# Optimization experiments

Measured on AMD Instinct MI355X. Metric: run time of the kernel, lower is better.

The kernel has to match this reference:

```python
import jax, jax.numpy as jnp
import numpy as np

B, T, F, H, A = 256, 256, 512, 1024, 1000
EPS = 1e-7  # keras CategoricalCrossentropy clip epsilon


def setup_inputs() -> dict:
    key = jax.random.key(0)
    ks = jax.random.split(key, 8)
    sF, sH = 1.0 / np.sqrt(F), 1.0 / np.sqrt(H)
    return {
        "inputs": jax.random.normal(ks[0], (B, T, F), dtype=jnp.float32),
        "Wx": jax.random.normal(ks[1], (F, H), dtype=jnp.float32) * sF,
        "Wh": jax.random.normal(ks[2], (H, H), dtype=jnp.float32) * sH,
        "b_rnn": jnp.zeros((H,), dtype=jnp.float32),
        "W1": jax.random.normal(ks[3], (H, H), dtype=jnp.float32) * sH,
        "b1": jnp.zeros((H,), dtype=jnp.float32),
        "W2": jax.random.normal(ks[4], (H, A), dtype=jnp.float32) * sH,
        "b2": jnp.zeros((A,), dtype=jnp.float32),
    }


def reference(inputs, Wx, Wh, b_rnn, W1, b1, W2, b2):
    # SimpleRNN with relu: h_t = relu(x_t @ Wx + h_{t-1} @ Wh + b)
    # Precompute the input projection as one big GEMM, then scan the recurrence.
    xw = jnp.einsum("btf,fh->bth", inputs, Wx) + b_rnn  # [B,T,H]

    def step(h, xw_t):
        h_new = jax.nn.relu(xw_t + h @ Wh)
        return h_new, None

    h0 = jnp.zeros((inputs.shape[0], Wh.shape[0]), dtype=inputs.dtype)
    h_last, _ = jax.lax.scan(step, h0, jnp.swapaxes(xw, 0, 1))  # scan over time

    hid = jax.nn.relu(h_last @ W1 + b1)                 # Dense relu
    probs = jax.nn.softmax(hid @ W2 + b2, axis=-1)      # Dense softmax -> [B,A]

    # tf.random.categorical receives the softmax *probabilities* but treats them
    # as unnormalized log-probs; we reproduce that faithfully with a fixed key.
    action = jax.random.categorical(jax.random.key(42), probs, axis=-1)
    action = action.astype(jnp.int32)

    # CategoricalCrossentropy(one_hot(action), probs), mean over batch
    targets = jax.nn.one_hot(action, probs.shape[-1], dtype=probs.dtype)
    p = jnp.clip(probs, EPS, 1.0 - EPS)
    loss = -jnp.mean(jnp.sum(targets * jnp.log(p), axis=-1))
    return action, loss
```

## Files before the change

kernel.cpp:

```cpp
#include <hip/hip_runtime.h>
#include <hip/hip_bf16.h>

#define B_ 256
#define T_ 256
#define F_ 512
#define H_ 1024
#define A_ 1000
#define EPS_ 1e-7f

typedef __hip_bfloat16 bf16;

__global__ __launch_bounds__(256) void detect_kernel(
    const unsigned* __restrict__ wx_words, int* __restrict__ flag)
{
    __shared__ int cnt[256];
    const int tid = threadIdx.x;
    int c = 0;
    for (int k = tid; k < 65536; k += 256) {
        unsigned lo = wx_words[k] & 0xFFFFu;
        unsigned e = (lo >> 7) & 0xFFu;
        if (e >= 105u && e <= 126u) c++;
    }
    cnt[tid] = c;
    __syncthreads();
    for (int s = 128; s > 0; s >>= 1) {
        if (tid < s) cnt[tid] += cnt[tid + s];
        __syncthreads();
    }
    if (tid == 0) flag[0] = (cnt[0] > 32768) ? 1 : 0;
}

__device__ __forceinline__ float load_maybe(const void* p, long i, int isbf16)
{
    return isbf16 ? __bfloat162float(((const bf16*)p)[i])
                  : ((const float*)p)[i];
}

__global__ __launch_bounds__(256) void gemm_kernel(
    const void* __restrict__ A1, int a1_maybe, long a1_off, int lda1, int K1,
    const float* __restrict__ A2, int lda2, int K2,
    const void* __restrict__ Wa, const void* __restrict__ Wb,
    const void* __restrict__ bias,
    const int* __restrict__ flagp,
    float* __restrict__ C, int M, int N, int do_relu)
{
    const int flagv = flagp[0];
    const int a1_bf = a1_maybe ? flagv : 0;

    __shared__ float As[32][33];
    __shared__ float Bs[32][33];

    const int tid = threadIdx.x;
    const int tx = tid & 15;
    const int ty = tid >> 4;
    const int n0 = blockIdx.x * 32;
    const int m0 = blockIdx.y * 32;

    float acc00 = 0.f, acc01 = 0.f, acc10 = 0.f, acc11 = 0.f;

    for (int part = 0; part < 2; ++part) {
        const void* Wp = part ? Wb : Wa;
        const int    K = part ? K2 : K1;
        if (part == 1 && (A2 == nullptr || K2 <= 0)) continue;

        for (int k0 = 0; k0 < K; k0 += 32) {
            #pragma unroll
            for (int i = 0; i < 4; ++i) {
                int idx = tid + i * 256;
                int r = idx >> 5, c = idx & 31;
                float av;
                if (part == 0) {
                    long off = a1_off + (long)(m0 + r) * lda1 + (k0 + c);
                    av = load_maybe(A1, off, a1_bf);
                } else {
                    av = A2[(long)(m0 + r) * lda2 + (k0 + c)];
                }
                As[r][c] = av;
                int n = n0 + c;
                Bs[r][c] = (n < N) ? load_maybe(Wp, (long)(k0 + r) * N + n, flagv)
                                   : 0.0f;
            }
            __syncthreads();
            #pragma unroll
            for (int k = 0; k < 32; ++k) {
                float a0 = As[ty * 2][k];
                float a1 = As[ty * 2 + 1][k];
                float b0 = Bs[k][tx * 2];
                float b1 = Bs[k][tx * 2 + 1];
                acc00 = fmaf(a0, b0, acc00); acc01 = fmaf(a0, b1, acc01);
                acc10 = fmaf(a1, b0, acc10); acc11 = fmaf(a1, b1, acc11);
            }
            __syncthreads();
        }
    }

    const int m = m0 + ty * 2;
    const int n = n0 + tx * 2;
    float bs0 = (n     < N) ? load_maybe(bias, n,     flagv) : 0.0f;
    float bs1 = (n + 1 < N) ? load_maybe(bias, n + 1, flagv) : 0.0f;
    float v00 = acc00 + bs0, v01 = acc01 + bs1;
    float v10 = acc10 + bs0, v11 = acc11 + bs1;
    if (do_relu) {
        v00 = fmaxf(v00, 0.f); v01 = fmaxf(v01, 0.f);
        v10 = fmaxf(v10, 0.f); v11 = fmaxf(v11, 0.f);
    }
    if (n     < N) C[(long)m * N + n]           = v00;
    if (n + 1 < N) C[(long)m * N + n + 1]       = v01;
    if (n     < N) C[(long)(m + 1) * N + n]     = v10;
    if (n + 1 < N) C[(long)(m + 1) * N + n + 1] = v11;
}

__global__ __launch_bounds__(256, 2) void xw_gemm_kernel(
    const void* __restrict__ X,
    const void* __restrict__ Wx,
    const void* __restrict__ brnn,
    const int* __restrict__ flagp,
    float* __restrict__ C,
    int t0)
{
    const int flagv = flagp[0];
    __shared__ float As[16][132];
    __shared__ float Bs[16][132];

    const int tid = threadIdx.x;
    const int tx = tid & 15;
    const int ty = tid >> 4;
    const int n0 = blockIdx.x * 128;
    const int m0 = blockIdx.y * 128;

    float acc[8][8] = {{0.f}};

    for (int k0 = 0; k0 < F_; k0 += 16) {
        #pragma unroll
        for (int i = 0; i < 8; ++i) {
            int idx = tid + i * 256;
            int ka = idx & 15, r = idx >> 4;
            int rg = m0 + r;
            long irow = (long)(rg >> 5) * 256 + t0 + (rg & 31);
            As[ka][r] = load_maybe(X, irow * F_ + k0 + ka, flagv);
            int nb = idx & 127, kb = idx >> 7;
            Bs[kb][nb] = load_maybe(Wx, (long)(k0 + kb) * H_ + n0 + nb, flagv);
        }
        __syncthreads();
        #pragma unroll
        for (int k = 0; k < 16; ++k) {
            float4 a0 = *(const float4*)&As[k][ty * 4];
            float4 a1 = *(const float4*)&As[k][ty * 4 + 64];
            float4 b0 = *(const float4*)&Bs[k][tx * 4];
            float4 b1 = *(const float4*)&Bs[k][tx * 4 + 64];
            float av[8] = {a0.x, a0.y, a0.z, a0.w, a1.x, a1.y, a1.z, a1.w};
            float bv[8] = {b0.x, b0.y, b0.z, b0.w, b1.x, b1.y, b1.z, b1.w};
            #pragma unroll
            for (int i = 0; i < 8; ++i)
                #pragma unroll
                for (int j = 0; j < 8; ++j)
                    acc[i][j] = fmaf(av[i], bv[j], acc[i][j]);
        }
        __syncthreads();
    }

    float bb[8];
    #pragma unroll
    for (int j = 0; j < 8; ++j) {
        int n = n0 + tx * 4 + (j & 3) + (j >> 2) * 64;
        bb[j] = load_maybe(brnn, n, flagv);
    }
    #pragma unroll
    for (int i = 0; i < 8; ++i) {
        int m = m0 + ty * 4 + (i & 3) + (i >> 2) * 64;
        float4 v0 = {acc[i][0] + bb[0], acc[i][1] + bb[1],
                     acc[i][2] + bb[2], acc[i][3] + bb[3]};
        float4 v1 = {acc[i][4] + bb[4], acc[i][5] + bb[5],
                     acc[i][6] + bb[6], acc[i][7] + bb[7]};
        *(float4*)&C[(long)m * H_ + n0 + tx * 4]      = v0;
        *(float4*)&C[(long)m * H_ + n0 + tx * 4 + 64] = v1;
    }
}

__global__ __launch_bounds__(256) void convert_wh_kernel(
    const void* __restrict__ Wh, const int* __restrict__ flagp,
    float* __restrict__ whf)
{
    const int flagv = flagp[0];
    long i = (long)blockIdx.x * 256 + threadIdx.x;
    whf[i] = load_maybe(Wh, i, flagv);
}

__global__ __launch_bounds__(1024) void rnn_step2_kernel(
    const float* __restrict__ hT,
    const float* __restrict__ Wh,
    const float* __restrict__ xw,
    float* __restrict__ hTn)
{
    const int tid  = threadIdx.x;
    const int lane = tid & 63;
    const int w    = __builtin_amdgcn_readfirstlane(tid >> 6);
    const int g    = w & 3;
    const int q    = w >> 2;
    const int m    = blockIdx.y * 64 + lane;
    const int n0   = blockIdx.x * 16 + g * 4;

    const float* __restrict__ ap = hT + ((long)q << 16) + m;
    const float* __restrict__ bp = Wh + ((long)q << 18) + n0;

    float acc0 = 0.f, acc1 = 0.f, acc2 = 0.f, acc3 = 0.f;
    #pragma unroll 8
    for (int k = 0; k < 256; ++k) {
        float  a = ap[(long)k << 8];
        float4 b = *(const float4*)(bp + ((long)k << 10));
        acc0 = fmaf(a, b.x, acc0);
        acc1 = fmaf(a, b.y, acc1);
        acc2 = fmaf(a, b.z, acc2);
        acc3 = fmaf(a, b.w, acc3);
    }

    __shared__ float4 part[3][4][64];
    if (q > 0) part[q - 1][g][lane] = make_float4(acc0, acc1, acc2, acc3);
    __syncthreads();

    if (q == 0) {
        float4 p0 = part[0][g][lane];
        float4 p1 = part[1][g][lane];
        float4 p2 = part[2][g][lane];
        const float4 xv = *(const float4*)(xw + (long)m * (32 * 1024) + n0);
        float s0 = ((acc0 + p0.x) + p1.x) + p2.x;
        float s1 = ((acc1 + p0.y) + p1.y) + p2.y;
        float s2 = ((acc2 + p0.z) + p1.z) + p2.z;
        float s3 = ((acc3 + p0.w) + p1.w) + p2.w;
        float v0 = fmaxf(s0 + xv.x, 0.f);
        float v1 = fmaxf(s1 + xv.y, 0.f);
        float v2 = fmaxf(s2 + xv.z, 0.f);
        float v3 = fmaxf(s3 + xv.w, 0.f);
        hTn[(long)(n0 + 0) * 256 + m] = v0;
        hTn[(long)(n0 + 1) * 256 + m] = v1;
        hTn[(long)(n0 + 2) * 256 + m] = v2;
        hTn[(long)(n0 + 3) * 256 + m] = v3;
    }
}

__global__ __launch_bounds__(256) void transpose_kernel(
    const float* __restrict__ in,
    float* __restrict__ out)
{
    __shared__ float t[32][33];
    const int tid = threadIdx.x;
    const int c  = tid & 31;
    const int r8 = tid >> 5;
    const int x0 = blockIdx.x * 32;
    const int y0 = blockIdx.y * 32;
    #pragma unroll
    for (int i = 0; i < 4; ++i) {
        int r = r8 + i * 8;
        t[r][c] = in[(long)(x0 + r) * 256 + y0 + c];
    }
    __syncthreads();
    #pragma unroll
    for (int i = 0; i < 4; ++i) {
        int r = r8 + i * 8;
        out[(long)(y0 + r) * 1024 + x0 + c] = t[c][r];
    }
}

__device__ __forceinline__ unsigned rotl32(unsigned v, int r) {
    return (v << r) | (v >> (32 - r));
}

__device__ __forceinline__ void threefry2x32(unsigned k0, unsigned k1,
                                             unsigned x0, unsigned x1,
                                             unsigned& o0, unsigned& o1)
{
    unsigned ks2 = k0 ^ k1 ^ 0x1BD11BDAu;
    x0 += k0; x1 += k1;
#define R4(ra, rb, rc, rd)                              \
    x0 += x1; x1 = rotl32(x1, ra); x1 ^= x0;            \
    x0 += x1; x1 = rotl32(x1, rb); x1 ^= x0;            \
    x0 += x1; x1 = rotl32(x1, rc); x1 ^= x0;            \
    x0 += x1; x1 = rotl32(x1, rd); x1 ^= x0;
    R4(13, 15, 26, 6);  x0 += k1;  x1 += ks2 + 1u;
    R4(17, 29, 16, 24); x0 += ks2; x1 += k0  + 2u;
    R4(13, 15, 26, 6);  x0 += k0;  x1 += k1  + 3u;
    R4(17, 29, 16, 24); x0 += k1;  x1 += ks2 + 4u;
    R4(13, 15, 26, 6);  x0 += ks2; x1 += k0  + 5u;
#undef R4
    o0 = x0; o1 = x1;
}

__device__ __forceinline__ float gumbel_at(unsigned j)
{
    unsigned o0, o1;
    threefry2x32(0u, 42u, 0u, j, o0, o1);
    unsigned bits = o0 ^ o1;
    unsigned ub = (bits >> 9) | 0x3F800000u;
    float u = __uint_as_float(ub) - 1.0f;
    const float TINY = 1.1754943508222875e-38f;
    u = fmaxf(TINY, u * (1.0f - TINY) + TINY);
    return -logf(-logf(u));
}

__global__ __launch_bounds__(256) void sample_kernel(
    const float* __restrict__ logits,
    float* __restrict__ out,
    float* __restrict__ loss_acc)
{
    const int b = blockIdx.x;
    const int tid = threadIdx.x;
    const float* row = logits + (long)b * A_;

    __shared__ float sv[256];
    __shared__ int   si[256];

    float lv[4];
    float lmax = -INFINITY;
    #pragma unroll
    for (int i = 0; i < 4; ++i) {
        int a = tid + i * 256;
        lv[i] = (a < A_) ? row[a] : -INFINITY;
        lmax = fmaxf(lmax, lv[i]);
    }
    sv[tid] = lmax;
    __syncthreads();
    for (int s = 128; s > 0; s >>= 1) {
        if (tid < s) sv[tid] = fmaxf(sv[tid], sv[tid + s]);
        __syncthreads();
    }
    lmax = sv[0];
    __syncthreads();

    float e[4];
    float lsum = 0.f;
    #pragma unroll
    for (int i = 0; i < 4; ++i) {
        int a = tid + i * 256;
        e[i] = (a < A_) ? expf(lv[i] - lmax) : 0.0f;
        lsum += e[i];
    }
    sv[tid] = lsum;
    __syncthreads();
    for (int s = 128; s > 0; s >>= 1) {
        if (tid < s) sv[tid] += sv[tid + s];
        __syncthreads();
    }
    const float inv = 1.0f / sv[0];
    __syncthreads();

    float bestv = -INFINITY;
    int   besti = 500;
    #pragma unroll
    for (int i = 0; i < 4; ++i) {
        int a = tid + i * 256;
        if (a < A_) {
            float score = e[i] * inv + gumbel_at((unsigned)(b * A_ + a));
            if (score > bestv) { bestv = score; besti = a; }
        }
    }
    sv[tid] = bestv; si[tid] = besti;
    __syncthreads();
    for (int s = 128; s > 0; s >>= 1) {
        if (tid < s) {
            float v2 = sv[tid + s]; int i2 = si[tid + s];
            if (v2 > sv[tid] || (v2 == sv[tid] && i2 < si[tid])) {
                sv[tid] = v2; si[tid] = i2;
            }
        }
        __syncthreads();
    }

    if (tid == 0) {
        int act = si[0];
        out[b] = (float)act;
        float p = expf(row[act] - lmax) * inv;
        p = fminf(fmaxf(p, EPS_), 1.0f - EPS_);
        atomicAdd(loss_acc, -logf(p) * (1.0f / (float)B_));
    }
}

__global__ void finalize_kernel(const float* __restrict__ loss_acc,
                                float* __restrict__ out)
{
    out[B_] = *loss_acc;
}

extern "C" void kernel_launch(void* const* d_in, const int* in_sizes, int n_in,
                              void* d_out, int out_size, void* d_ws, size_t ws_size,
                              hipStream_t stream)
{
    (void)out_size;

    const void *inputs = nullptr, *Wx = nullptr, *Wh = nullptr, *b_rnn = nullptr,
               *W1 = nullptr, *b1 = nullptr, *W2 = nullptr, *b2 = nullptr;
    for (int i = 0; i < n_in; ++i) {
        int s = in_sizes[i];
        if      (s == 33554432) inputs = d_in[i];
        else if (s == 524288)   Wx = d_in[i];
        else if (s == 1048576)  { if (!Wh) Wh = d_in[i]; else W1 = d_in[i]; }
        else if (s == 1024)     { if (!b_rnn) b_rnn = d_in[i]; else b1 = d_in[i]; }
        else if (s == 1024000)  W2 = d_in[i];
        else if (s == 1000)     b2 = d_in[i];
    }
    if (!inputs) inputs = d_in[0];
    if (!Wx) Wx = d_in[1];  if (!Wh) Wh = d_in[2];  if (!b_rnn) b_rnn = d_in[3];
    if (!W1) W1 = d_in[4];  if (!b1) b1 = d_in[5];  if (!W2) W2 = d_in[6];
    if (!b2) b2 = d_in[7];

    float* out = (float*)d_out;
    float* ws = (float*)d_ws;

    dim3 blk(256);
    dim3 grdH((H_ + 31) / 32, B_ / 32);
    dim3 grdA((A_ + 31) / 32, B_ / 32);

    const size_t XW_FLOATS = (size_t)8192 * 1024;
    const size_t need_floats = XW_FLOATS + 2 * 262144 + 1048576
                             + 262144 + 262144 + 256000 + 2;
    if (ws_size >= need_floats * sizeof(float)) {
        float* xwbuf    = ws;
        float* hT0      = xwbuf + XW_FLOATS;
        float* hT1      = hT0 + 262144;
        float* whf      = hT1 + 262144;
        float* hlast    = whf + 1048576;
        float* hid      = hlast + 262144;
        float* logits   = hid + 262144;
        float* loss_acc = logits + 256000;
        int*   flag     = (int*)(loss_acc + 1);

        hipMemsetAsync(hT0, 0, 262144 * sizeof(float), stream);
        hipMemsetAsync(loss_acc, 0, sizeof(float), stream);

        detect_kernel<<<1, blk, 0, stream>>>((const unsigned*)Wx, flag);
        convert_wh_kernel<<<4096, blk, 0, stream>>>(Wh, flag, whf);

        float* hp = hT0;
        float* hn = hT1;
        for (int c = 0; c < 8; ++c) {
            xw_gemm_kernel<<<dim3(8, 64), blk, 0, stream>>>(
                inputs, Wx, b_rnn, flag, xwbuf, c * 32);
            for (int tl = 0; tl < 32; ++tl) {
                rnn_step2_kernel<<<dim3(64, 4), dim3(1024), 0, stream>>>(
                    hp, whf, xwbuf + (long)tl * 1024, hn);
                float* tmp = hp; hp = hn; hn = tmp;
            }
        }

        transpose_kernel<<<dim3(32, 8), blk, 0, stream>>>(hp, hlast);

        gemm_kernel<<<grdH, blk, 0, stream>>>(
            hlast, 0, 0, H_, H_, nullptr, 0, 0, W1, nullptr, b1, flag,
            hid, B_, H_, 1);
        gemm_kernel<<<grdA, blk, 0, stream>>>(
            hid, 0, 0, H_, H_, nullptr, 0, 0, W2, nullptr, b2, flag,
            logits, B_, A_, 0);

        sample_kernel<<<dim3(B_), blk, 0, stream>>>(logits, out, loss_acc);
        finalize_kernel<<<1, 1, 0, stream>>>(loss_acc, out);
        return;
    }

    float* hA       = ws;
    float* hB       = hA + (long)B_ * H_;
    float* hid      = hB + (long)B_ * H_;
    float* logits   = hid + (long)B_ * H_;
    float* loss_acc = logits + (long)B_ * A_;
    int*   flag     = (int*)(loss_acc + 1);

    hipMemsetAsync(hA, 0, (size_t)B_ * H_ * sizeof(float), stream);
    hipMemsetAsync(loss_acc, 0, sizeof(float), stream);

    detect_kernel<<<1, blk, 0, stream>>>((const unsigned*)Wx, flag);

    float* hp = hA;
    float* hn = hB;
    for (int t = 0; t < T_; ++t) {
        gemm_kernel<<<grdH, blk, 0, stream>>>(
            inputs, 1, (long)t * F_, T_ * F_, F_,
            hp, H_, H_,
            Wx, Wh, b_rnn, flag,
            hn, B_, H_, 1);
        float* tmp = hp; hp = hn; hn = tmp;
    }

    gemm_kernel<<<grdH, blk, 0, stream>>>(
        hp, 0, 0, H_, H_, nullptr, 0, 0, W1, nullptr, b1, flag, hid, B_, H_, 1);
    gemm_kernel<<<grdA, blk, 0, stream>>>(
        hid, 0, 0, H_, H_, nullptr, 0, 0, W2, nullptr, b2, flag, logits, B_, A_, 0);

    sample_kernel<<<dim3(B_), blk, 0, stream>>>(logits, out, loss_acc);
    finalize_kernel<<<1, 1, 0, stream>>>(loss_acc, out);
}
```

Before: 5.401 ms.

## Restructure RNN step kernel to split K across 16 waves with wider batch tiles

Replaces the per-step recurrence kernel with a variant in which each block covers 64 hidden outputs by 16 batch rows. The K dimension is split across 16 wavefronts of 64 each, so every thread keeps 16 accumulators and loads one Wh value per k, with the hidden-state values broadcast as float4s. Partial sums are reduced through shared memory, then bias, ReLU and the transposed store are applied. The aim is to raise FMA-to-load ratio and Wh reuse per step, at the cost of a 16-way shared-memory reduction and a strided global write.

Measured after the change: 7.078 ms. 31.1% more time.

```diff
diff --git a/kernel.cpp b/kernel.cpp
--- a/kernel.cpp
+++ b/kernel.cpp
@@ -186,56 +186,71 @@
     whf[i] = load_maybe(Wh, i, flagv);
 }
 
-__global__ __launch_bounds__(1024) void rnn_step2_kernel(
+__global__ __launch_bounds__(1024) void rnn_step3_kernel(
     const float* __restrict__ hT,
     const float* __restrict__ Wh,
     const float* __restrict__ xw,
     float* __restrict__ hTn)
 {
+    __shared__ float part[16][64][16];
+
     const int tid  = threadIdx.x;
     const int lane = tid & 63;
-    const int w    = __builtin_amdgcn_readfirstlane(tid >> 6);
-    const int g    = w & 3;
-    const int q    = w >> 2;
-    const int m    = blockIdx.y * 64 + lane;
-    const int n0   = blockIdx.x * 16 + g * 4;
-
-    const float* __restrict__ ap = hT + ((long)q << 16) + m;
-    const float* __restrict__ bp = Wh + ((long)q << 18) + n0;
-
-    float acc0 = 0.f, acc1 = 0.f, acc2 = 0.f, acc3 = 0.f;
-    #pragma unroll 8
-    for (int k = 0; k < 256; ++k) {
-        float  a = ap[(long)k << 8];
-        float4 b = *(const float4*)(bp + ((long)k << 10));
-        acc0 = fmaf(a, b.x, acc0);
-        acc1 = fmaf(a, b.y, acc1);
-        acc2 = fmaf(a, b.z, acc2);
-        acc3 = fmaf(a, b.w, acc3);
-    }
-
-    __shared__ float4 part[3][4][64];
-    if (q > 0) part[q - 1][g][lane] = make_float4(acc0, acc1, acc2, acc3);
-    __syncthreads();
-
-    if (q == 0) {
-        float4 p0 = part[0][g][lane];
-        float4 p1 = part[1][g][lane];
-        float4 p2 = part[2][g][lane];
-        const float4 xv = *(const float4*)(xw + (long)m * (32 * 1024) + n0);
-        float s0 = ((acc0 + p0.x) + p1.x) + p2.x;
-        float s1 = ((acc1 + p0.y) + p1.y) + p2.y;
-        float s2 = ((acc2 + p0.z) + p1.z) + p2.z;
-        float s3 = ((acc3 + p0.w) + p1.w) + p2.w;
-        float v0 = fmaxf(s0 + xv.x, 0.f);
-        float v1 = fmaxf(s1 + xv.y, 0.f);
-        float v2 = fmaxf(s2 + xv.z, 0.f);
-        float v3 = fmaxf(s3 + xv.w, 0.f);
-        hTn[(long)(n0 + 0) * 256 + m] = v0;
-        hTn[(long)(n0 + 1) * 256 + m] = v1;
-        hTn[(long)(n0 + 2) * 256 + m] = v2;
-        hTn[(long)(n0 + 3) * 256 + m] = v3;
-    }
+    const int q    = __builtin_amdgcn_readfirstlane(tid >> 6);
+    const int n    = blockIdx.x * 64 + lane;
+    const int m0   = blockIdx.y * 16;
+
+    const float* __restrict__ wp = Wh + ((long)q << 6) * H_ + n;
+    const float* __restrict__ hp = hT + ((long)q << 6) * B_ + m0;
+
+    float acc[16];
+    #pragma unroll
+    for (int i = 0; i < 16; ++i) acc[i] = 0.f;
+
+    #pragma unroll 4
+    for (int k = 0; k < 64; ++k) {
+        float wv = wp[(long)k << 10];
+        const float4* hv = (const float4*)(hp + ((long)k << 8));
+        float4 h0 = hv[0];
+        float4 h1 = hv[1];
+        float4 h2 = hv[2];
+        float4 h3 = hv[3];
+        acc[0]  = fmaf(h0.x, wv, acc[0]);
+        acc[1]  = fmaf(h0.y, wv, acc[1]);
+        acc[2]  = fmaf(h0.z, wv, acc[2]);
+        acc[3]  = fmaf(h0.w, wv, acc[3]);
+        acc[4]  = fmaf(h1.x, wv, acc[4]);
+        acc[5]  = fmaf(h1.y, wv, acc[5]);
+        acc[6]  = fmaf(h1.z, wv, acc[6]);
+        acc[7]  = fmaf(h1.w, wv, acc[7]);
+        acc[8]  = fmaf(h2.x, wv, acc[8]);
+        acc[9]  = fmaf(h2.y, wv, acc[9]);
+        acc[10] = fmaf(h2.z, wv, acc[10]);
+        acc[11] = fmaf(h2.w, wv, acc[11]);
+        acc[12] = fmaf(h3.x, wv, acc[12]);
+        acc[13] = fmaf(h3.y, wv, acc[13]);
+        acc[14] = fmaf(h3.z, wv, acc[14]);
+        acc[15] = fmaf(h3.w, wv, acc[15]);
+    }
+
+    #pragma unroll
+    for (int i = 0; i < 4; ++i) {
+        *(float4*)&part[q][lane][i * 4] =
+            make_float4(acc[i * 4], acc[i * 4 + 1], acc[i * 4 + 2], acc[i * 4 + 3]);
+    }
+    __syncthreads();
+
+    const int n_out = tid >> 4;
+    const int mi    = tid & 15;
+    float s = part[0][n_out][mi];
+    #pragma unroll
+    for (int qq = 1; qq < 16; ++qq) s += part[qq][n_out][mi];
+
+    const int gm = m0 + mi;
+    const int gn = blockIdx.x * 64 + n_out;
+    const float xv = xw[(long)gm * (32 * 1024) + gn];
+    const float v  = fmaxf(s + xv, 0.f);
+    hTn[(long)gn * 256 + gm] = v;
 }
 
 __global__ __launch_bounds__(256) void transpose_kernel(
@@ -435,7 +450,7 @@
             xw_gemm_kernel<<<dim3(8, 64), blk, 0, stream>>>(
                 inputs, Wx, b_rnn, flag, xwbuf, c * 32);
             for (int tl = 0; tl < 32; ++tl) {
-                rnn_step2_kernel<<<dim3(64, 4), dim3(1024), 0, stream>>>(
+                rnn_step3_kernel<<<dim3(16, 16), dim3(1024), 0, stream>>>(
                     hp, whf, xwbuf + (long)tl * 1024, hn);
                 float* tmp = hp; hp = hn; hn = tmp;
             }
```
